# Kernel tuning notes

Hardware: AMD Instinct MI355X
Metric: run time of the kernel (lower is better)

## Reference

```python
import jax, jax.numpy as jnp
import numpy as np

N_QUBITS = 12
K_STEPS = 6
VOCAB = 32000
D_EMB = 512
N_CLASSES = 8
B = 256
SEQ = 128
DIM = 2 ** N_QUBITS


def apply_1q(psi, U, q):
    # psi: [B, 2^n]; U: [2,2] (shared) or [B,2,2] (per-sample). Apply on wire q
    # (PennyLane convention: wire 0 = most significant axis).
    b = psi.shape[0]
    left, right = 2 ** q, 2 ** (N_QUBITS - q - 1)
    st = psi.reshape(b, left, 2, right)
    if U.ndim == 3:
        st = jnp.einsum('bij,bajr->bair', U, st)
    else:
        st = jnp.einsum('ij,bajr->bair', U, st)
    return st.reshape(b, DIM)


def apply_cnot(psi, c, t):
    b = psi.shape[0]
    st = psi.reshape((b,) + (2,) * N_QUBITS)
    c_ax, t_ax = 1 + c, 1 + t
    c0 = jnp.take(st, 0, axis=c_ax)
    c1 = jnp.take(st, 1, axis=c_ax)
    t_ax2 = t_ax - 1 if t_ax > c_ax else t_ax  # axis shift after take
    c1 = jnp.flip(c1, axis=t_ax2)
    return jnp.stack([c0, c1], axis=c_ax).reshape(b, DIM)


def ry_mat(angle):
    # angle: [B] -> [B,2,2] complex64
    c = jnp.cos(angle / 2)
    s = jnp.sin(angle / 2)
    row0 = jnp.stack([c, -s], axis=-1)
    row1 = jnp.stack([s, c], axis=-1)
    return jnp.stack([row0, row1], axis=-2).astype(jnp.complex64)


def rot_mat(phi, theta, omega):
    # PennyLane Rot(phi, theta, omega) = RZ(omega) RY(theta) RZ(phi)
    c = jnp.cos(theta / 2)
    s = jnp.sin(theta / 2)
    ep = jnp.exp(-0.5j * (phi + omega).astype(jnp.complex64))
    em = jnp.exp(0.5j * (phi - omega).astype(jnp.complex64))
    m = jnp.stack([jnp.stack([ep * c, -em * s]), jnp.stack([jnp.conj(em) * s, jnp.conj(ep) * c])])
    return m.astype(jnp.complex64)


def block(psi, x, theta_k):
    # data reupload RY(x_i), trainable Rot, ring of CNOTs (noiseless)
    for i in range(N_QUBITS):
        psi = apply_1q(psi, ry_mat(x[:, i]), i)
    for i in range(N_QUBITS):
        psi = apply_1q(psi, rot_mat(theta_k[i, 0], theta_k[i, 1], theta_k[i, 2]), i)
    for i in range(N_QUBITS - 1):
        psi = apply_cnot(psi, i, i + 1)
    psi = apply_cnot(psi, N_QUBITS - 1, 0)
    return psi


def z_expvals(psi):
    # <Z_i> for all wires from |psi|^2
    b = psi.shape[0]
    p = (psi.real ** 2 + psi.imag ** 2).reshape((b,) + (2,) * N_QUBITS)
    zs = []
    for i in range(N_QUBITS):
        axes = tuple(ax for ax in range(1, N_QUBITS + 1) if ax != 1 + i)
        m = p.sum(axis=axes)  # [B,2]
        zs.append(m[:, 0] - m[:, 1])
    return jnp.stack(zs, axis=-1)  # [B, n_qubits]


def _forward(input_ids, attention_mask, emb_table, proj_w, proj_b, theta, head_w, head_b):
    # encoder: embed -> masked mean pool -> tanh(linear) * pi
    e = emb_table[input_ids]                              # [B,S,D]
    mask = attention_mask[:, :, None].astype(jnp.float32)
    pooled = (e * mask).sum(axis=1) / jnp.clip(mask.sum(axis=1), 1.0)
    x = jnp.tanh(pooled @ proj_w.T + proj_b) * jnp.float32(np.pi)  # [B, n_qubits]

    b = x.shape[0]
    psi = jnp.zeros((b, DIM), jnp.complex64).at[:, 0].set(1.0)
    readouts = []
    for k in range(K_STEPS):
        psi = block(psi, x, theta[k])
        readouts.append(z_expvals(psi))
    step_readouts = jnp.stack(readouts, axis=0)           # [K,B,n_qubits]
    step_logits = step_readouts @ head_w.T + head_b       # [K,B,n_classes]
    return step_logits, step_readouts, step_logits[-1]


def setup_inputs() -> dict:
    key = jax.random.key(0)
    ks = jax.random.split(key, 6)
    input_ids = jax.random.randint(ks[0], (B, SEQ), 0, VOCAB)
    attention_mask = jnp.ones((B, SEQ), dtype=jnp.int32)
    emb_table = jax.random.normal(ks[1], (VOCAB, D_EMB), jnp.float32)
    emb_table = emb_table.at[0].set(0.0)  # padding_idx=0 row is zeros
    proj_w = jax.random.normal(ks[2], (N_QUBITS, D_EMB), jnp.float32) / np.sqrt(D_EMB)
    proj_b = jnp.zeros((N_QUBITS,), jnp.float32)
    theta = 0.01 * jax.random.normal(ks[3], (K_STEPS, N_QUBITS, 3), jnp.float32)
    head_w = jax.random.normal(ks[4], (N_CLASSES, N_QUBITS), jnp.float32) / np.sqrt(N_QUBITS)
    head_b = jnp.zeros((N_CLASSES,), jnp.float32)
    return {'input_ids': input_ids, 'attention_mask': attention_mask,
            'emb_table': emb_table, 'proj_w': proj_w, 'proj_b': proj_b,
            'theta': theta, 'head_w': head_w, 'head_b': head_b}


def reference(input_ids, attention_mask, emb_table, proj_w, proj_b, theta, head_w, head_b):
    return _forward(input_ids, attention_mask, emb_table, proj_w, proj_b, theta, head_w, head_b)
```

## Files before the change

kernel.cpp:

```cpp
#include <hip/hip_runtime.h>
#include <math.h>

#define NQ 12
#define DIM 4096
#define KS 6
#define BB 256
#define SEQ 128
#define DEMB 512


#define RG(P, W) { \
    float4 c0 = *(const float4*)&s_u[k][W][0]; \
    float4 c1 = *(const float4*)&s_u[k][W][4]; \
    float u00r=c0.x,u00i=c0.y,u01r=c0.z,u01i=c0.w; \
    float u10r=c1.x,u10i=c1.y,u11r=c1.z,u11i=c1.w; \
    _Pragma("unroll") \
    for (int r0 = 0; r0 < 4; ++r0) if (!(r0 & (1 << (P)))) { \
        int r1 = r0 | (1 << (P)); \
        float2 A = a[r0], Bv = a[r1]; \
        a[r0].x = u00r*A.x - u00i*A.y + u01r*Bv.x - u01i*Bv.y; \
        a[r0].y = u00r*A.y + u00i*A.x + u01r*Bv.y + u01i*Bv.x; \
        a[r1].x = u10r*A.x - u10i*A.y + u11r*Bv.x - u11i*Bv.y; \
        a[r1].y = u10r*A.y + u10i*A.x + u11r*Bv.y + u11i*Bv.x; \
    } }

#define BF_PLAIN(v, m) { float p_ = __shfl_xor(v, m, 64); v = v + p_; }
#define BF_SIGN(v, m)  { float p_ = __shfl_xor(v, m, 64); float d_ = v - p_; \
                         v = (lane & m) ? -d_ : d_; }

#define WAVE_FENCE() asm volatile("s_waitcnt lgkmcnt(0)" ::: "memory")

__device__ __forceinline__ int swz14(int x) { return x ^ ((x >> 4) & 14); }

__global__ __launch_bounds__(1024) void fused_kernel(
    const int* __restrict__ ids, const int* __restrict__ mask,
    const float* __restrict__ emb, const float* __restrict__ pw,
    const float* __restrict__ pb, const float* __restrict__ theta,
    const float* __restrict__ hw, const float* __restrict__ hb,
    float* __restrict__ readouts, float* __restrict__ logits,
    float* __restrict__ last)
{
    __shared__ __align__(16) float2 buf0[DIM];
    __shared__ __align__(16) float2 buf1[DIM];
    __shared__ __align__(16) float2 buf2[DIM];
    __shared__ __align__(16) float  s_u[KS][NQ][8];
    __shared__ float  s_red[16][NQ];
    __shared__ float  s_msum[8];
    __shared__ float  s_wred[2][NQ];
    __shared__ float  s_x[NQ];
    __shared__ float  s_hw[8 * NQ];
    __shared__ float  s_hb[8];

    int b = blockIdx.x;
    int tid = threadIdx.x;
    int lane = tid & 63, wave = tid >> 6;

    int*   s_ids = (int*)buf1;
    float* s_m   = (float*)buf1 + SEQ;
    float4* s_part = (float4*)buf0;

    if (tid < SEQ) {
        s_ids[tid] = ids[b * SEQ + tid];
        s_m[tid]   = (float)mask[b * SEQ + tid];
    }
    if (tid >= 256 && tid < 256 + 8 * NQ) s_hw[tid - 256] = hw[tid - 256];
    if (tid >= 384 && tid < 392)          s_hb[tid - 384] = hb[tid - 384];
    __syncthreads();

    {
        int g = tid >> 7, e = tid & 127;
        float4 acc = make_float4(0.f, 0.f, 0.f, 0.f);
        float msum = 0.f;
        #pragma unroll 4
        for (int s = g; s < SEQ; s += 8) {
            float m = s_m[s];
            float4 v = ((const float4*)emb)[(size_t)s_ids[s] * 128 + e];
            acc.x = fmaf(m, v.x, acc.x);
            acc.y = fmaf(m, v.y, acc.y);
            acc.z = fmaf(m, v.z, acc.z);
            acc.w = fmaf(m, v.w, acc.w);
            msum += m;
        }
        __syncthreads();
        s_part[g * 128 + e] = acc;
        if (e == 0) s_msum[g] = msum;
    }
    __syncthreads();

    if (tid < 128) {
        float tm = s_msum[0] + s_msum[1] + s_msum[2] + s_msum[3]
                 + s_msum[4] + s_msum[5] + s_msum[6] + s_msum[7];
        tm = fmaxf(tm, 1.f);
        float inv = 1.f / tm;
        float4 p = make_float4(0.f, 0.f, 0.f, 0.f);
        #pragma unroll
        for (int g = 0; g < 8; ++g) {
            float4 pg = s_part[g * 128 + tid];
            p.x += pg.x; p.y += pg.y; p.z += pg.z; p.w += pg.w;
        }
        p.x *= inv; p.y *= inv; p.z *= inv; p.w *= inv;
        float z[NQ];
        #pragma unroll
        for (int i = 0; i < NQ; ++i) {
            float4 w4 = ((const float4*)pw)[i * 128 + tid];
            z[i] = p.x * w4.x + p.y * w4.y + p.z * w4.z + p.w * w4.w;
        }
        #pragma unroll
        for (int i = 0; i < NQ; ++i) {
            #pragma unroll
            for (int off = 32; off > 0; off >>= 1)
                z[i] += __shfl_xor(z[i], off, 64);
        }
        if ((tid & 63) == 0) {
            int w = tid >> 6;
            #pragma unroll
            for (int i = 0; i < NQ; ++i) s_wred[w][i] = z[i];
        }
    }
    __syncthreads();
    if (tid < NQ) {
        float d = pb[tid] + s_wred[0][tid] + s_wred[1][tid];
        s_x[tid] = tanhf(d) * 3.14159274101257324f;
    }
    __syncthreads();

    if (tid < KS * NQ) {
        int k = tid / NQ, w = tid % NQ;
        float ang = s_x[w];
        float cy = cosf(0.5f * ang), sy = sinf(0.5f * ang);
        const float* th = theta + (k * NQ + w) * 3;
        float phi = th[0], te = th[1], om = th[2];
        float ct = cosf(0.5f * te), st = sinf(0.5f * te);
        float a1 = -0.5f * (phi + om);
        float epr = cosf(a1), epi = sinf(a1);
        float a2 = 0.5f * (phi - om);
        float emr = cosf(a2), emi = sinf(a2);
        float R00r = epr * ct,  R00i = epi * ct;
        float R01r = -emr * st, R01i = -emi * st;
        float R10r = emr * st,  R10i = -emi * st;
        float R11r = epr * ct,  R11i = -epi * ct;
        s_u[k][w][0] =  R00r * cy + R01r * sy;
        s_u[k][w][1] =  R00i * cy + R01i * sy;
        s_u[k][w][2] = -R00r * sy + R01r * cy;
        s_u[k][w][3] = -R00i * sy + R01i * cy;
        s_u[k][w][4] =  R10r * cy + R11r * sy;
        s_u[k][w][5] =  R10i * cy + R11i * sy;
        s_u[k][w][6] = -R10r * sy + R11r * cy;
        s_u[k][w][7] = -R10i * sy + R11i * cy;
    }

    int T4 = tid << 2;
    int bA4 = swz14(T4) >> 1;
    int aB[4], aC[4], aD[4], aE[4], aF[4], idxP[4];
    #pragma unroll
    for (int r = 0; r < 4; ++r) {
        aB[r] = swz14((wave << 8) | ((lane >> 2) << 4) | (r << 2) | (lane & 3));
        aC[r] = swz14((wave << 8) | ((lane >> 4) << 6) | (r << 4) | (lane & 15));
        aD[r] = swz14((wave << 8) | (r << 6) | lane);
        aE[r] = swz14(((lane >> 4) << 10) | (r << 8) | (wave << 4) | (lane & 15));
        int jF = (r << 10) | ((lane >> 4) << 8) | (wave << 4) | (lane & 15);
        aF[r] = swz14(jF);
        int b0 = (jF >> 11) & 1;
        int pref = b0, outv = 0;
        for (int w = 1; w < NQ; ++w) {
            pref ^= (jF >> (11 - w)) & 1;
            outv |= pref << (11 - w);
        }
        outv |= (b0 ^ pref) << 11;
        idxP[r] = swz14(outv);
    }
    int s3v   = (wave >> 3) & 1;
    int s32v  = s3v ^ ((wave >> 2) & 1);
    int s321v = s32v ^ ((wave >> 1) & 1);
    int sallv = s321v ^ (wave & 1);

    float2 a[4];
    #pragma unroll
    for (int r = 0; r < 4; ++r) a[r] = make_float2(0.f, 0.f);
    if (tid == 0) a[0].x = 1.f;
    __syncthreads();

    for (int k = 0; k < KS; ++k) {
        RG(0, 11) RG(1, 10)

        #pragma unroll
        for (int i = 0; i < 2; ++i)
            ((float4*)buf0)[bA4 ^ i] =
                make_float4(a[2*i].x, a[2*i].y, a[2*i+1].x, a[2*i+1].y);
        WAVE_FENCE();
        #pragma unroll
        for (int r = 0; r < 4; ++r) a[r] = buf0[aB[r]];

        RG(0, 9) RG(1, 8)

        #pragma unroll
        for (int r = 0; r < 4; ++r) buf0[aB[r]] = a[r];
        WAVE_FENCE();
        #pragma unroll
        for (int r = 0; r < 4; ++r) a[r] = buf0[aC[r]];

        RG(0, 7) RG(1, 6)

        #pragma unroll
        for (int r = 0; r < 4; ++r) buf0[aC[r]] = a[r];
        WAVE_FENCE();
        #pragma unroll
        for (int r = 0; r < 4; ++r) a[r] = buf0[aD[r]];

        RG(0, 5) RG(1, 4)

        #pragma unroll
        for (int r = 0; r < 4; ++r) buf0[aD[r]] = a[r];
        __syncthreads();
        #pragma unroll
        for (int r = 0; r < 4; ++r) a[r] = buf0[aE[r]];

        RG(0, 3) RG(1, 2)

        #pragma unroll
        for (int r = 0; r < 4; ++r) buf1[aE[r]] = a[r];
        WAVE_FENCE();
        #pragma unroll
        for (int r = 0; r < 4; ++r) a[r] = buf1[aF[r]];

        RG(0, 1) RG(1, 0)

        #pragma unroll
        for (int r = 0; r < 4; ++r) buf2[idxP[r]] = a[r];

        {
            float p0 = a[0].x*a[0].x + a[0].y*a[0].y;
            float p1 = a[1].x*a[1].x + a[1].y*a[1].y;
            float p2 = a[2].x*a[2].x + a[2].y*a[2].y;
            float p3 = a[3].x*a[3].x + a[3].y*a[3].y;
            float T1v = (p0 + p3) - (p1 + p2);
            float T0v = (p0 + p2) - (p1 + p3);

            float v1 = T1v;
            BF_PLAIN(v1,32) BF_PLAIN(v1,16) BF_PLAIN(v1,8)
            BF_PLAIN(v1,4)  BF_PLAIN(v1,2)  BF_PLAIN(v1,1)

            float c = T1v;
            BF_SIGN(c,32);
            float w2v = c; BF_PLAIN(w2v,16) BF_PLAIN(w2v,8) BF_PLAIN(w2v,4)
                           BF_PLAIN(w2v,2)  BF_PLAIN(w2v,1)
            BF_SIGN(c,16);
            float w3v = c; BF_PLAIN(w3v,8) BF_PLAIN(w3v,4)
                           BF_PLAIN(w3v,2) BF_PLAIN(w3v,1)
            BF_SIGN(c,8);
            float w8v = c; BF_PLAIN(w8v,4) BF_PLAIN(w8v,2) BF_PLAIN(w8v,1)
            BF_SIGN(c,4);
            float w9v = c; BF_PLAIN(w9v,2) BF_PLAIN(w9v,1)
            BF_SIGN(c,2);
            float w10v = c; BF_PLAIN(w10v,1)
            BF_SIGN(c,1);

            float q0 = T0v;
            BF_SIGN(q0,32) BF_SIGN(q0,16) BF_SIGN(q0,8)
            BF_SIGN(q0,4)  BF_SIGN(q0,2)  BF_SIGN(q0,1)

            if (lane == 0) {
                float* sr = s_red[wave];
                sr[0]  = sallv ? -q0   : q0;
                sr[1]  = v1;
                sr[2]  = w2v;
                sr[3]  = w3v;
                sr[4]  = s3v   ? -w3v  : w3v;
                sr[5]  = s32v  ? -w3v  : w3v;
                sr[6]  = s321v ? -w3v  : w3v;
                sr[7]  = sallv ? -w3v  : w3v;
                sr[8]  = sallv ? -w8v  : w8v;
                sr[9]  = sallv ? -w9v  : w9v;
                sr[10] = sallv ? -w10v : w10v;
                sr[11] = sallv ? -c    : c;
            }
        }

        __syncthreads();
        #pragma unroll
        for (int i = 0; i < 2; ++i) {
            float4 v = ((float4*)buf2)[bA4 ^ i];
            a[2*i]   = make_float2(v.x, v.y);
            a[2*i+1] = make_float2(v.z, v.w);
        }

        if (tid < NQ) {
            float s = 0.f;
            #pragma unroll
            for (int w2 = 0; w2 < 16; ++w2) s += s_red[w2][tid];
            readouts[(k * BB + b) * NQ + tid] = s;
        }
        if (tid < 8) {
            float acc2 = s_hb[tid];
            #pragma unroll
            for (int i = 0; i < NQ; ++i) {
                float si = 0.f;
                #pragma unroll
                for (int w2 = 0; w2 < 16; ++w2) si += s_red[w2][i];
                acc2 = fmaf(si, s_hw[tid * NQ + i], acc2);
            }
            logits[(k * BB + b) * 8 + tid] = acc2;
            if (k == KS - 1) last[b * 8 + tid] = acc2;
        }
    }
}

extern "C" void kernel_launch(void* const* d_in, const int* in_sizes, int n_in,
                              void* d_out, int out_size, void* d_ws, size_t ws_size,
                              hipStream_t stream) {
    const int*   ids   = (const int*)d_in[0];
    const int*   mask  = (const int*)d_in[1];
    const float* emb   = (const float*)d_in[2];
    const float* pw    = (const float*)d_in[3];
    const float* pb    = (const float*)d_in[4];
    const float* theta = (const float*)d_in[5];
    const float* hw    = (const float*)d_in[6];
    const float* hb    = (const float*)d_in[7];
    float* out = (float*)d_out;

    float* readouts = out + KS * BB * 8;
    float* last     = out + KS * BB * 8 + KS * BB * NQ;

    fused_kernel<<<BB, 1024, 0, stream>>>(ids, mask, emb, pw, pb, theta,
                                          hw, hb, readouts, out, last);
}
```

Measured before the change: 143.9 us.

## Replace intra-wave LDS transposes with shuffle-based register swaps

Qubit-axis transposes that stay inside one wavefront now use __shfl_xor pair swaps instead of writing to and reading back from shared memory. This drops one LDS buffer and the wave fences between those stages. The per-gate matrix setup is also spread over four threads per entry instead of one. Each swap still costs two cross-lane shuffles plus selects, so total data movement through the cross-lane path stays comparable, and the register layout must match exactly what the later LDS stages and readout expect.

```diff
diff --git a/kernel.cpp b/kernel.cpp
--- a/kernel.cpp
+++ b/kernel.cpp
@@ -24,11 +24,18 @@
         a[r1].y = u10r*A.y + u10i*A.x + u11r*Bv.y + u11i*Bv.x; \
     } }
 
+#define SWAPB(lo, hi, M) { \
+    float tx_ = (lane & M) ? lo.x : hi.x; \
+    float ty_ = (lane & M) ? lo.y : hi.y; \
+    tx_ = __shfl_xor(tx_, M, 64); \
+    ty_ = __shfl_xor(ty_, M, 64); \
+    if (lane & M) { lo.x = tx_; lo.y = ty_; } \
+    else          { hi.x = tx_; hi.y = ty_; } \
+}
+
 #define BF_PLAIN(v, m) { float p_ = __shfl_xor(v, m, 64); v = v + p_; }
 #define BF_SIGN(v, m)  { float p_ = __shfl_xor(v, m, 64); float d_ = v - p_; \
                          v = (lane & m) ? -d_ : d_; }
-
-#define WAVE_FENCE() asm volatile("s_waitcnt lgkmcnt(0)" ::: "memory")
 
 __device__ __forceinline__ int swz14(int x) { return x ^ ((x >> 4) & 14); }
 
@@ -41,7 +48,6 @@
     float* __restrict__ last)
 {
     __shared__ __align__(16) float2 buf0[DIM];
-    __shared__ __align__(16) float2 buf1[DIM];
     __shared__ __align__(16) float2 buf2[DIM];
     __shared__ __align__(16) float  s_u[KS][NQ][8];
     __shared__ float  s_red[16][NQ];
@@ -55,8 +61,8 @@
     int tid = threadIdx.x;
     int lane = tid & 63, wave = tid >> 6;
 
-    int*   s_ids = (int*)buf1;
-    float* s_m   = (float*)buf1 + SEQ;
+    int*   s_ids = (int*)buf2;
+    float* s_m   = (float*)buf2 + SEQ;
     float4* s_part = (float4*)buf0;
 
     if (tid < SEQ) {
@@ -124,42 +130,34 @@
     }
     __syncthreads();
 
-    if (tid < KS * NQ) {
-        int k = tid / NQ, w = tid % NQ;
+    if (tid < KS * NQ * 4) {
+        int k = tid / 48;
+        int rem = tid - k * 48;
+        int w = rem >> 2, q = rem & 3;
         float ang = s_x[w];
         float cy = cosf(0.5f * ang), sy = sinf(0.5f * ang);
         const float* th = theta + (k * NQ + w) * 3;
         float phi = th[0], te = th[1], om = th[2];
         float ct = cosf(0.5f * te), st = sinf(0.5f * te);
         float a1 = -0.5f * (phi + om);
-        float epr = cosf(a1), epi = sinf(a1);
-        float a2 = 0.5f * (phi - om);
-        float emr = cosf(a2), emi = sinf(a2);
-        float R00r = epr * ct,  R00i = epi * ct;
-        float R01r = -emr * st, R01i = -emi * st;
-        float R10r = emr * st,  R10i = -emi * st;
-        float R11r = epr * ct,  R11i = -epi * ct;
-        s_u[k][w][0] =  R00r * cy + R01r * sy;
-        s_u[k][w][1] =  R00i * cy + R01i * sy;
-        s_u[k][w][2] = -R00r * sy + R01r * cy;
-        s_u[k][w][3] = -R00i * sy + R01i * cy;
-        s_u[k][w][4] =  R10r * cy + R11r * sy;
-        s_u[k][w][5] =  R10i * cy + R11i * sy;
-        s_u[k][w][6] = -R10r * sy + R11r * cy;
-        s_u[k][w][7] = -R10i * sy + R11i * cy;
+        float a2 =  0.5f * (phi - om);
+        float ar =  cosf(a1) * ct, ai =  sinf(a1) * ct;
+        float br = -cosf(a2) * st, bi = -sinf(a2) * st;
+        float x1 = (q & 1) ? ai : ar;
+        float x2 = (q & 1) ? bi : br;
+        float E  = (q & 2) ? (x2 * cy - x1 * sy) : (x1 * cy + x2 * sy);
+        s_u[k][w][q] = E;
+        s_u[k][w][(q & 2) ? q + 2 : q + 6] = (q == 1 || q == 2) ? -E : E;
     }
 
     int T4 = tid << 2;
     int bA4 = swz14(T4) >> 1;
-    int aB[4], aC[4], aD[4], aE[4], aF[4], idxP[4];
+    int aD[4], aE[4], idxP[4];
     #pragma unroll
     for (int r = 0; r < 4; ++r) {
-        aB[r] = swz14((wave << 8) | ((lane >> 2) << 4) | (r << 2) | (lane & 3));
-        aC[r] = swz14((wave << 8) | ((lane >> 4) << 6) | (r << 4) | (lane & 15));
         aD[r] = swz14((wave << 8) | (r << 6) | lane);
         aE[r] = swz14(((lane >> 4) << 10) | (r << 8) | (wave << 4) | (lane & 15));
         int jF = (r << 10) | ((lane >> 4) << 8) | (wave << 4) | (lane & 15);
-        aF[r] = swz14(jF);
         int b0 = (jF >> 11) & 1;
         int pref = b0, outv = 0;
         for (int w = 1; w < NQ; ++w) {
@@ -183,29 +181,18 @@
     for (int k = 0; k < KS; ++k) {
         RG(0, 11) RG(1, 10)
 
-        #pragma unroll
-        for (int i = 0; i < 2; ++i)
-            ((float4*)buf0)[bA4 ^ i] =
-                make_float4(a[2*i].x, a[2*i].y, a[2*i+1].x, a[2*i+1].y);
-        WAVE_FENCE();
-        #pragma unroll
-        for (int r = 0; r < 4; ++r) a[r] = buf0[aB[r]];
+        SWAPB(a[0], a[1], 1) SWAPB(a[2], a[3], 1)
+        SWAPB(a[0], a[2], 2) SWAPB(a[1], a[3], 2)
 
         RG(0, 9) RG(1, 8)
 
-        #pragma unroll
-        for (int r = 0; r < 4; ++r) buf0[aB[r]] = a[r];
-        WAVE_FENCE();
-        #pragma unroll
-        for (int r = 0; r < 4; ++r) a[r] = buf0[aC[r]];
+        SWAPB(a[0], a[1], 4) SWAPB(a[2], a[3], 4)
+        SWAPB(a[0], a[2], 8) SWAPB(a[1], a[3], 8)
 
         RG(0, 7) RG(1, 6)
 
-        #pragma unroll
-        for (int r = 0; r < 4; ++r) buf0[aC[r]] = a[r];
-        WAVE_FENCE();
-        #pragma unroll
-        for (int r = 0; r < 4; ++r) a[r] = buf0[aD[r]];
+        SWAPB(a[0], a[1], 16) SWAPB(a[2], a[3], 16)
+        SWAPB(a[0], a[2], 32) SWAPB(a[1], a[3], 32)
 
         RG(0, 5) RG(1, 4)
 
@@ -217,11 +204,8 @@
 
         RG(0, 3) RG(1, 2)
 
-        #pragma unroll
-        for (int r = 0; r < 4; ++r) buf1[aE[r]] = a[r];
-        WAVE_FENCE();
-        #pragma unroll
-        for (int r = 0; r < 4; ++r) a[r] = buf1[aF[r]];
+        SWAPB(a[0], a[1], 16) SWAPB(a[2], a[3], 16)
+        SWAPB(a[0], a[2], 32) SWAPB(a[1], a[3], 32)
 
         RG(0, 1) RG(1, 0)
 
```

New measurement: 146.6 us. About the same (+1.9%).
